# Kernel tuning notes

Measured on AMD Instinct MI355X. Metric: run time of the kernel, lower is better.

The kernel has to match this reference:

```python
import jax, jax.numpy as jnp
import numpy as np

G, K = 4, 3
P = K * K  # n_offset_points


def _conv(x, w, b, groups=1):
    # x: [B,C,H,W] NCHW, w: [O, I/groups, kh, kw] (torch OIHW), padding=1 -> SAME
    y = jax.lax.conv_general_dilated(x, w, (1, 1), 'SAME', feature_group_count=groups)
    return y + b[None, :, None, None]


def setup_inputs() -> dict:
    key = jax.random.key(0)
    ks = jax.random.split(key, 9)
    B, C, H, W = 4, 256, 64, 64
    Cg = C // G
    s = 0.05
    return {
        'x': jax.random.normal(ks[0], (B, H * W, C), jnp.float32),
        'off_w1': jax.random.normal(ks[1], (C, Cg, 3, 3), jnp.float32) * s,
        'off_b1': jax.random.normal(ks[2], (C,), jnp.float32) * s,
        'off_w2': jax.random.normal(ks[3], (G * 2 * P, C, 3, 3), jnp.float32) * s,
        'off_b2': jax.random.normal(ks[4], (G * 2 * P,), jnp.float32) * s,
        'mod_w1': jax.random.normal(ks[5], (C // 4, C, 3, 3), jnp.float32) * s,
        'mod_b1': jax.random.normal(ks[6], (C // 4,), jnp.float32) * s,
        'mod_w2': jax.random.normal(ks[7], (G * P, C // 4, 3, 3), jnp.float32) * s,
        'mod_b2': jax.random.normal(ks[8], (G * P,), jnp.float32) * s,
        'H': 64,
        'W': 64,
    }


def reference(x, off_w1, off_b1, off_w2, off_b2, mod_w1, mod_b1, mod_w2, mod_b2, H, W):
    B, N, C = x.shape
    Cg = C // G
    x2d = x.transpose(0, 2, 1).reshape(B, C, H, W)

    # offset branch (grouped 3x3 conv -> GELU -> 3x3 conv), offset_scale = 1.0
    h = jax.nn.gelu(_conv(x2d, off_w1, off_b1, groups=G), approximate=False)
    off = _conv(h, off_w2, off_b2).reshape(B, G, 2, P, H, W)
    # modulation branch
    m = jax.nn.gelu(_conv(x2d, mod_w1, mod_b1), approximate=False)
    mod = jax.nn.sigmoid(_conv(m, mod_w2, mod_b2)).reshape(B, G, P, H, W)

    # base kernel offsets: base[0]=x, base[1]=y, each [P]
    rv = jnp.arange(-(K - 1) // 2, (K - 1) // 2 + 1, dtype=x.dtype)
    by, bx = jnp.meshgrid(rv, rv, indexing='ij')
    bx, by = bx.reshape(P), by.reshape(P)

    yg, xg = jnp.meshgrid(jnp.arange(H, dtype=x.dtype), jnp.arange(W, dtype=x.dtype), indexing='ij')
    # sampling coords in pixel space; clamp to [-1,1] normalized (align_corners=True)
    # is exactly clamp to [0, W-1] / [0, H-1] in pixel space, and border padding
    # then never goes out of range.
    px = jnp.clip(xg + bx[:, None, None] + off[:, :, 0], 0.0, W - 1)  # [B,G,P,H,W]
    py = jnp.clip(yg + by[:, None, None] + off[:, :, 1], 0.0, H - 1)

    x0f, y0f = jnp.floor(px), jnp.floor(py)
    wx, wy = px - x0f, py - y0f
    x0 = x0f.astype(jnp.int32)
    y0 = y0f.astype(jnp.int32)
    x1 = jnp.minimum(x0 + 1, W - 1)
    y1 = jnp.minimum(y0 + 1, H - 1)

    flat = x2d.reshape(B, G, Cg, H * W)

    def gather(yi, xi):
        idx = (yi * W + xi).reshape(B, G, 1, P, H * W)
        return jnp.take_along_axis(flat[:, :, :, None, :], idx, axis=-1)  # [B,G,Cg,P,HW]

    wxr = wx.reshape(B, G, 1, P, H * W)
    wyr = wy.reshape(B, G, 1, P, H * W)
    v = (gather(y0, x0) * (1 - wxr) * (1 - wyr)
         + gather(y0, x1) * wxr * (1 - wyr)
         + gather(y1, x0) * (1 - wxr) * wyr
         + gather(y1, x1) * wxr * wyr)
    v = v * mod.reshape(B, G, 1, P, H * W)
    out = v.mean(axis=3)  # average over offset points -> [B,G,Cg,HW]
    return out.reshape(B, C, H * W).transpose(0, 2, 1)
```

## Files before the change

### kernel.cpp

```cpp
#include <hip/hip_runtime.h>
#include <math.h>


#define SLAB 4369
#define AGAP 1056
#define APXS 40
#define AROW (66*APXS)

typedef __attribute__((ext_vector_type(8))) short short8;
typedef __attribute__((ext_vector_type(4))) float floatx4;

__device__ __forceinline__ unsigned short f2bf(float f) {
    unsigned u = __float_as_uint(f);
    u = (u + 0x7FFFu + ((u >> 16) & 1u)) >> 16;
    return (unsigned short)u;
}
__device__ __forceinline__ float bf2f(unsigned short h) {
    return __uint_as_float(((unsigned)h) << 16);
}
__device__ __forceinline__ void split2(float v, unsigned short* hi, unsigned short* lo) {
    unsigned short h = f2bf(v);
    *hi = h;
    *lo = f2bf(v - bf2f(h));
}
__device__ __forceinline__ float gelu_exact(float v) {
    return 0.5f * v * (1.0f + erff(v * 0.70710678118654752f));
}

template<int NC, int TG, int MT, int NT, int ACT, int OUTMODE>
__device__ __forceinline__ void conv_core_lds(
    unsigned short* lds,
    const unsigned short* __restrict__ ah, const unsigned short* __restrict__ al,
    int aC0,
    const unsigned short* __restrict__ wh, const unsigned short* __restrict__ wl,
    int wC0,
    const float* __restrict__ bias,
    int b, int mblock, int tap0,
    unsigned short* __restrict__ oh, unsigned short* __restrict__ ol,
    int oC0,
    float* __restrict__ pf)
{
    const int OCPAD = NT * 16;
    const int NSTG = NC * TG;
    const int AHALF_ = MT * AROW;
    const int AU = MT * 66 * 4;
    const int KA = (AU + 255) / 256;
    const int BHALF_ = 3 * OCPAD * APXS;
    const int BU = 3 * OCPAD * 4;
    const int KB = (BU + 255) / 256;

    unsigned short* Ahl = lds;
    unsigned short* All = lds + AHALF_;
    unsigned short* Bhl = lds + 2 * AHALF_;
    unsigned short* Bll = Bhl + BHALF_;

    int tid = (int)threadIdx.x;
    int wave = tid >> 6;
    int lane = tid & 63;
    int quad = lane >> 4;
    int l16 = lane & 15;

    int pix0 = (mblock * 4 + wave) * (MT * 16);
    int y0 = mblock * MT;
    int lr = (MT == 4) ? wave : (wave >> 1);
    int xb_ = (MT == 4) ? 0 : ((wave & 1) * 32);

    floatx4 acc[MT][NT];
#pragma unroll
    for (int nt = 0; nt < NT; nt++) {
        float bv = (OUTMODE == 1) ? bias[nt * 16 + l16] : 0.f;
#pragma unroll
        for (int mt = 0; mt < MT; mt++) { floatx4 v = {bv, bv, bv, bv}; acc[mt][nt] = v; }
    }

    short8 ARh[KA], ARl[KA], BRh[KB], BRl[KB];

    auto issueAB = [&](int s) {
        int ch = s / TG;
        int kh = (TG == 3) ? (s % 3) : (tap0 / 3);
        size_t ga = ((size_t)((aC0 + ch) * 4 + b) * SLAB + (size_t)(y0 + kh) * 66) * 32;
#pragma unroll
        for (int k = 0; k < KA; k++) {
            int u = k * 256 + tid;
            if (u < AU) {
                ARh[k] = *(const short8*)(ah + ga + (size_t)u * 8);
                ARl[k] = *(const short8*)(al + ga + (size_t)u * 8);
            }
        }
        size_t gb = ((size_t)((wC0 + ch) * 9 + kh * 3)) * OCPAD * 32;
#pragma unroll
        for (int k = 0; k < KB; k++) {
            int u = k * 256 + tid;
            if (u < BU) {
                BRh[k] = *(const short8*)(wh + gb + (size_t)u * 8);
                BRl[k] = *(const short8*)(wl + gb + (size_t)u * 8);
            }
        }
    };
    auto writeAB = [&]() {
#pragma unroll
        for (int k = 0; k < KA; k++) {
            int u = k * 256 + tid;
            if (u < AU) {
                int px = u >> 2, j = u & 3;
                int row = px / 66, col = px - row * 66;
                int dst = row * AROW + col * APXS + j * 8;
                *(short8*)(Ahl + dst) = ARh[k];
                *(short8*)(All + dst) = ARl[k];
            }
        }
#pragma unroll
        for (int k = 0; k < KB; k++) {
            int u = k * 256 + tid;
            if (u < BU) {
                int tp = u / (OCPAD * 4);
                int r = u - tp * (OCPAD * 4);
                int oc = r >> 2, j = u & 3;
                int dst = tp * (OCPAD * APXS) + oc * APXS + j * 8;
                *(short8*)(Bhl + dst) = BRh[k];
                *(short8*)(Bll + dst) = BRl[k];
            }
        }
    };

    issueAB(0);
    writeAB();
    __syncthreads();

#pragma unroll 1
    for (int s = 0; s < NSTG; s++) {
        if (s + 1 < NSTG) {
            issueAB(s + 1);
            __builtin_amdgcn_sched_barrier(0);
        }
#pragma unroll
        for (int kw = 0; kw < 3; kw++) {
            short8 Afh[MT], Afl[MT], Bfh[NT], Bfl[NT];
#pragma unroll
            for (int mt = 0; mt < MT; mt++) {
                int aoff = lr * AROW + (xb_ + kw + l16 + mt * 16) * APXS + quad * 8;
                Afh[mt] = *(const short8*)(Ahl + aoff);
                Afl[mt] = *(const short8*)(All + aoff);
            }
#pragma unroll
            for (int nt = 0; nt < NT; nt++) {
                int boff = kw * (OCPAD * APXS) + (nt * 16 + l16) * APXS + quad * 8;
                Bfh[nt] = *(const short8*)(Bhl + boff);
                Bfl[nt] = *(const short8*)(Bll + boff);
            }
            __builtin_amdgcn_s_setprio(1);
#pragma unroll
            for (int nt = 0; nt < NT; nt++) {
#pragma unroll
                for (int mt = 0; mt < MT; mt++) {
                    acc[mt][nt] = __builtin_amdgcn_mfma_f32_16x16x32_bf16(Afh[mt], Bfh[nt], acc[mt][nt], 0, 0, 0);
                    acc[mt][nt] = __builtin_amdgcn_mfma_f32_16x16x32_bf16(Afh[mt], Bfl[nt], acc[mt][nt], 0, 0, 0);
                    acc[mt][nt] = __builtin_amdgcn_mfma_f32_16x16x32_bf16(Afl[mt], Bfh[nt], acc[mt][nt], 0, 0, 0);
                }
            }
            __builtin_amdgcn_s_setprio(0);
        }
        if (s + 1 < NSTG) {
            __syncthreads();
            writeAB();
            __syncthreads();
        }
    }

#pragma unroll
    for (int nt = 0; nt < NT; nt++) {
        int oc = nt * 16 + l16;
#pragma unroll
        for (int mt = 0; mt < MT; mt++) {
#pragma unroll
            for (int r = 0; r < 4; r++) {
                float v = acc[mt][nt][r];
                int px = pix0 + mt * 16 + quad * 4 + r;
                if (OUTMODE == 2) {
                    atomicAdd(pf + ((size_t)b * 4096 + px) * OCPAD + oc, v);
                } else if (OUTMODE == 3) {
                    pf[((size_t)b * 4096 + px) * OCPAD + oc] = v;
                } else {
                    if (ACT == 1) v = gelu_exact(v);
                    else if (ACT == 2) v = 1.0f / (1.0f + expf(-v));
                    int yy = (px >> 6) + 1, xx = (px & 63) + 1;
                    int och = oC0 + (oc >> 5);
                    size_t o = ((size_t)(och * 4 + b) * SLAB + yy * 66 + xx) * 32 + (oc & 31);
                    unsigned short hv, lv; split2(v, &hv, &lv);
                    oh[o] = hv; ol[o] = lv;
                }
            }
        }
    }
}

__global__ __launch_bounds__(256, 1) void convA_kernel(
    const unsigned short* __restrict__ xph, const unsigned short* __restrict__ xpl,
    const unsigned short* __restrict__ w1h, const unsigned short* __restrict__ w1l,
    const float* __restrict__ off_b1,
    const unsigned short* __restrict__ w3h, const unsigned short* __restrict__ w3l,
    unsigned short* __restrict__ h1h, unsigned short* __restrict__ h1l,
    float* __restrict__ P3)
{
    __shared__ unsigned short lds[25920];
    int bx = blockIdx.x;
    int xcd = bx & 7;
    int j = bx >> 3;
    int pair = xcd * 16 + j / 7;
    int role = j % 7;
    int mb = pair & 31;
    int b = pair >> 5;
    if (role < 4) {
        int g = role;
        conv_core_lds<2, 3, 2, 4, 1, 1>(lds, xph, xpl, g * 2,
            w1h + (size_t)g * 2 * 9 * 64 * 32, w1l + (size_t)g * 2 * 9 * 64 * 32, 0,
            off_b1 + g * 64,
            b, mb, 0, h1h, h1l, g * 2, nullptr);
    } else {
        int ks = role - 4;
        conv_core_lds<8, 1, 2, 4, 0, 2>(lds, xph, xpl, 0,
            w3h, w3l, 0, nullptr,
            b, mb, ks * 3, nullptr, nullptr, 0, P3);
    }
}

__global__ __launch_bounds__(256) void finalizeA_kernel(
    const float* __restrict__ P3, const float* __restrict__ mod_b1,
    unsigned short* __restrict__ m1h, unsigned short* __restrict__ m1l)
{
    int idx = blockIdx.x * 256 + threadIdx.x;
    int c = idx & 63;
    int p = idx >> 6;
    int b = p >> 12;
    int px = p & 4095;
    int rem = ((px >> 6) + 1) * 66 + (px & 63) + 1;
    float u = P3[(size_t)p * 64 + c] + mod_b1[c];
    u = gelu_exact(u);
    size_t o = ((size_t)((c >> 5) * 4 + b) * SLAB + rem) * 32 + (c & 31);
    unsigned short hu, lu; split2(u, &hu, &lu);
    m1h[o] = hu; m1l[o] = lu;
}

__global__ __launch_bounds__(256, 1) void convB_kernel(
    const unsigned short* __restrict__ h1h, const unsigned short* __restrict__ h1l,
    const unsigned short* __restrict__ w2h, const unsigned short* __restrict__ w2l,
    const unsigned short* __restrict__ m1h, const unsigned short* __restrict__ m1l,
    const unsigned short* __restrict__ w4h, const unsigned short* __restrict__ w4l,
    float* __restrict__ P2a, float* __restrict__ P4a)
{
    __shared__ unsigned short lds[29760];
    int bx = blockIdx.x;
    int xcd = bx & 7;
    int j = bx >> 3;
    int pair = xcd * 16 + j / 4;
    int role = j % 4;
    int mb = pair & 31;
    int b = pair >> 5;
    if (role < 3) {
        conv_core_lds<8, 1, 2, 5, 0, 2>(lds, h1h, h1l, 0,
            w2h, w2l, 0, nullptr,
            b, mb, role * 3, nullptr, nullptr, 0, P2a);
    } else {
        conv_core_lds<2, 3, 2, 3, 0, 3>(lds, m1h, m1l, 0,
            w4h, w4l, 0, nullptr,
            b, mb, 0, nullptr, nullptr, 0, P4a);
    }
}

#define ZBLK 2304
#define RBLK 1040
#define XBLK 17424
#define WBLK 1980
__global__ void prep_all_kernel(
    const float* __restrict__ x,
    const float* __restrict__ w1f, const float* __restrict__ w2f,
    const float* __restrict__ w3f, const float* __restrict__ w4f,
    unsigned short* __restrict__ xph, unsigned short* __restrict__ xpl,
    unsigned short* __restrict__ h1h, unsigned short* __restrict__ h1l,
    unsigned short* __restrict__ m1h, unsigned short* __restrict__ m1l,
    unsigned short* __restrict__ w1h, unsigned short* __restrict__ w1l,
    unsigned short* __restrict__ w2h, unsigned short* __restrict__ w2l,
    unsigned short* __restrict__ w3h, unsigned short* __restrict__ w3l,
    unsigned short* __restrict__ w4h, unsigned short* __restrict__ w4l,
    float* __restrict__ accf)
{
    int blk = blockIdx.x;
    int t = threadIdx.x;
    if (blk < ZBLK) {
        ((uint4*)accf)[(size_t)blk * 256 + t] = make_uint4(0u, 0u, 0u, 0u);
        return;
    }
    blk -= ZBLK;
    if (blk < RBLK) {
        int b = blk / 260;
        int r = blk - b * 260;
        int i, j;
        if (r < 66)       { i = 0;        j = r; }
        else if (r < 132) { i = 65;       j = r - 66; }
        else if (r < 196) { i = r - 131;  j = 0; }
        else              { i = r - 195;  j = 65; }
        size_t pp = (size_t)i * 66 + j;
        int ch = t >> 5, sub = t & 31;
        size_t o = ((size_t)(ch * 4 + b) * SLAB + pp) * 32 + sub;
        h1h[o] = 0; h1l[o] = 0;
        if (t < 64) { m1h[o] = 0; m1l[o] = 0; }
        return;
    }
    blk -= RBLK;
    if (blk < XBLK) {
        int b = blk / 4356;
        int rem = blk - b * 4356;
        int i = rem / 66, j = rem - i * 66;
        float v = 0.f;
        if (i >= 1 && i <= 64 && j >= 1 && j <= 64)
            v = x[((size_t)b * 4096 + (size_t)(i - 1) * 64 + (j - 1)) * 256 + t];
        size_t o = ((size_t)((t >> 5) * 4 + b) * SLAB + rem) * 32 + (t & 31);
        unsigned short h, l; split2(v, &h, &l);
        xph[o] = h; xpl[o] = l;
        return;
    }
    blk -= XBLK;
    {
        const int N1 = 147456, N2 = 184320, N3 = 147456, N4 = 27648;
        int idx = blk * 256 + t;
        const float* w; unsigned short *outh, *outl;
        int ocpad, oc_real, ic, base;
        if (idx < N1)                { w = w1f; outh = w1h; outl = w1l; ocpad = 64; oc_real = 64; ic = 64;  base = 0; }
        else if (idx < N1 + N2)      { w = w2f; outh = w2h; outl = w2l; ocpad = 80; oc_real = 72; ic = 256; base = N1; }
        else if (idx < N1 + N2 + N3) { w = w3f; outh = w3h; outl = w3l; ocpad = 64; oc_real = 64; ic = 256; base = N1 + N2; }
        else                         { w = w4f; outh = w4h; outl = w4l; ocpad = 48; oc_real = 36; ic = 64;  base = N1 + N2 + N3; }
        int lidx = idx - base;
        int ici = lidx & 31;
        int t1 = lidx >> 5;
        int ocp = t1 % ocpad;
        int t2 = t1 / ocpad;
        int tap = t2 % 9;
        int t3 = t2 / 9;
        int nch = ic >> 5;
        int ch = t3 % nch;
        int g = t3 / nch;
        float v = 0.f;
        if (ocp < oc_real) {
            int oc = g * oc_real + ocp;
            int icx = ch * 32 + ici;
            v = w[((size_t)oc * ic + icx) * 9 + tap];
        }
        unsigned short h, l; split2(v, &h, &l);
        outh[lidx] = h; outl[lidx] = l;
    }
}

__global__ __launch_bounds__(256) void deform_sample(
    const float* __restrict__ x,
    const float* __restrict__ P2a, const float* __restrict__ P4a,
    const float* __restrict__ b2, const float* __restrict__ b4,
    float* __restrict__ out)
{
    int bid = (int)((blockIdx.x & 7u) * 512u + (blockIdx.x >> 3));
    int wid = (int)(((unsigned)bid * 256u + threadIdx.x) >> 6);
    int lane = (int)(threadIdx.x & 63u);
    int sub = lane >> 4;
    int li = lane & 15;

    int b = wid >> 12;
    int rem = wid & 4095;
    int g = rem >> 10;
    int hw = ((rem & 1023) << 2) + sub;
    int hy = hw >> 6;
    int wx = hw & 63;

    float fx = 0.f, fy = 0.f, fm = 0.f;
    if (li < 9) {
        size_t p = (size_t)(b << 12) + hw;
        int c2 = g * 18 + li;
        fx = P2a[p * 80 + c2] + b2[c2];
        fy = P2a[p * 80 + 9 + c2] + b2[9 + c2];
        int c4 = g * 9 + li;
        float mv = P4a[p * 48 + c4] + b4[c4];
        fm = 1.0f / (1.0f + expf(-mv));
    }
    float px = fminf(fmaxf((float)wx + (float)(li % 3 - 1) + fx, 0.f), 63.f);
    float py = fminf(fmaxf((float)hy + (float)(li / 3 - 1) + fy, 0.f), 63.f);
    float x0f = floorf(px), y0f = floorf(py);
    float wxf = px - x0f, wyf = py - y0f;
    int x0 = (int)x0f, y0 = (int)y0f;
    int x1 = min(x0 + 1, 63), y1 = min(y0 + 1, 63);

    const float4* xb = (const float4*)(x + ((size_t)(b << 12)) * 256 + g * 64 + li * 4);
    float4 acc = make_float4(0.f, 0.f, 0.f, 0.f);
    int sb = sub << 4;
#pragma unroll
    for (int q = 0; q < 9; q++) {
        int src = sb + q;
        int   qx0 = __shfl(x0, src);
        int   qx1 = __shfl(x1, src);
        int   qy0 = __shfl(y0, src);
        int   qy1 = __shfl(y1, src);
        float qwx = __shfl(wxf, src);
        float qwy = __shfl(wyf, src);
        float qm  = __shfl(fm, src);
        float4 v00 = xb[(size_t)(qy0 * 64 + qx0) * 64];
        float4 v01 = xb[(size_t)(qy0 * 64 + qx1) * 64];
        float4 v10 = xb[(size_t)(qy1 * 64 + qx0) * 64];
        float4 v11 = xb[(size_t)(qy1 * 64 + qx1) * 64];
        float w00 = (1.f - qwx) * (1.f - qwy);
        float w01 = qwx * (1.f - qwy);
        float w10 = (1.f - qwx) * qwy;
        float w11 = qwx * qwy;
        acc.x += qm * (v00.x * w00 + v01.x * w01 + v10.x * w10 + v11.x * w11);
        acc.y += qm * (v00.y * w00 + v01.y * w01 + v10.y * w10 + v11.y * w11);
        acc.z += qm * (v00.z * w00 + v01.z * w01 + v10.z * w10 + v11.z * w11);
        acc.w += qm * (v00.w * w00 + v01.w * w01 + v10.w * w10 + v11.w * w11);
    }
    const float s = 1.f / 9.f;
    acc.x *= s; acc.y *= s; acc.z *= s; acc.w *= s;
    float4* ob = (float4*)(out + ((size_t)(b << 12) + hw) * 256 + g * 64 + li * 4);
    *ob = acc;
}

extern "C" void kernel_launch(void* const* d_in, const int* in_sizes, int n_in,
                              void* d_out, int out_size, void* d_ws, size_t ws_size,
                              hipStream_t stream)
{
    const float* x      = (const float*)d_in[0];
    const float* off_w1 = (const float*)d_in[1];
    const float* off_b1 = (const float*)d_in[2];
    const float* off_w2 = (const float*)d_in[3];
    const float* off_b2 = (const float*)d_in[4];
    const float* mod_w1 = (const float*)d_in[5];
    const float* mod_b1 = (const float*)d_in[6];
    const float* mod_w2 = (const float*)d_in[7];
    const float* mod_b2 = (const float*)d_in[8];

    const size_t XP = 8u * 4u * SLAB * 32u;
    const size_t MP = 2u * 4u * SLAB * 32u;
    const size_t W1 = 4u * 2u * 9u * 64u * 32u;
    const size_t W2 = 8u * 9u * 80u * 32u;
    const size_t W3 = 8u * 9u * 64u * 32u;
    const size_t W4 = 2u * 9u * 48u * 32u;

    unsigned short* ws = (unsigned short*)d_ws;
    size_t o = 0;
    unsigned short* xph = ws + o; o += XP + AGAP;
    unsigned short* xpl = ws + o; o += XP + AGAP;
    unsigned short* h1h = ws + o; o += XP + AGAP;
    unsigned short* h1l = ws + o; o += XP + AGAP;
    unsigned short* m1h = ws + o; o += MP + AGAP;
    unsigned short* m1l = ws + o; o += MP + AGAP;
    unsigned short* w1h = ws + o; o += W1 + AGAP;
    unsigned short* w1l = ws + o; o += W1 + AGAP;
    unsigned short* w2h = ws + o; o += W2 + AGAP;
    unsigned short* w2l = ws + o; o += W2 + AGAP;
    unsigned short* w3h = ws + o; o += W3 + AGAP;
    unsigned short* w3l = ws + o; o += W3 + AGAP;
    unsigned short* w4h = ws + o; o += W4 + AGAP;
    unsigned short* w4l = ws + o; o += W4 + AGAP;
    o += o & 1;
    float* fbase = (float*)(ws + o);
    float* P3  = fbase;
    float* P2a = P3 + (size_t)4 * 4096 * 64;
    float* P4a = P2a + (size_t)4 * 4096 * 80;
    const size_t ACC_FLOATS = (size_t)4 * 4096 * (64 + 80 + 48);
    size_t need_bytes = o * 2 + ACC_FLOATS * 4;
    if (ws_size < need_bytes) return;

    prep_all_kernel<<<ZBLK + RBLK + XBLK + WBLK, 256, 0, stream>>>(
        x, off_w1, off_w2, mod_w1, mod_w2,
        xph, xpl, h1h, h1l, m1h, m1l,
        w1h, w1l, w2h, w2l, w3h, w3l, w4h, w4l, P3);

    convA_kernel<<<dim3(896, 1, 1), 256, 0, stream>>>(xph, xpl, w1h, w1l, off_b1,
                                                      w3h, w3l, h1h, h1l, P3);
    finalizeA_kernel<<<4096, 256, 0, stream>>>(P3, mod_b1, m1h, m1l);
    convB_kernel<<<dim3(512, 1, 1), 256, 0, stream>>>(h1h, h1l, w2h, w2l,
                                                      m1h, m1l, w4h, w4l, P2a, P4a);
    deform_sample<<<4096, 256, 0, stream>>>(x, P2a, P4a, off_b2, mod_b2, (float*)d_out);
}
```

Baseline: 190.2 us.

## Split convolutions over output channels instead of kernel rows, dropping atomics and finalize

The convolutions no longer split the 3x3 kernel rows across blocks and combine partial sums with fp32 atomics. Each block now covers all nine taps for a slice of output channels and writes its result directly, with bias and GELU fused in. This removes the accumulator zeroing in the prep kernel, the atomic traffic, and the separate finalize kernel, and shrinks the grids of both conv launches. In exchange, each block runs a longer serial K loop with fewer blocks in flight, which may lower occupancy and load balance.

```diff
diff --git a/kernel.cpp b/kernel.cpp
--- a/kernel.cpp
+++ b/kernel.cpp
@@ -27,7 +27,7 @@
     return 0.5f * v * (1.0f + erff(v * 0.70710678118654752f));
 }
 
-template<int NC, int TG, int MT, int NT, int ACT, int OUTMODE>
+template<int NC, int MT, int NT, int OCW, int OSTRF, int ACT, int OUTMODE>
 __device__ __forceinline__ void conv_core_lds(
     unsigned short* lds,
     const unsigned short* __restrict__ ah, const unsigned short* __restrict__ al,
@@ -35,18 +35,19 @@
     const unsigned short* __restrict__ wh, const unsigned short* __restrict__ wl,
     int wC0,
     const float* __restrict__ bias,
-    int b, int mblock, int tap0,
+    int b, int mblock,
     unsigned short* __restrict__ oh, unsigned short* __restrict__ ol,
     int oC0,
-    float* __restrict__ pf)
-{
-    const int OCPAD = NT * 16;
-    const int NSTG = NC * TG;
+    float* __restrict__ pf,
+    int oc0)
+{
+    const int NSTG = NC * 3;
     const int AHALF_ = MT * AROW;
     const int AU = MT * 66 * 4;
     const int KA = (AU + 255) / 256;
-    const int BHALF_ = 3 * OCPAD * APXS;
-    const int BU = 3 * OCPAD * 4;
+    const int BHALF_ = 3 * NT * 16 * APXS;
+    const int UB1 = NT * 64;
+    const int BU = 3 * UB1;
     const int KB = (BU + 255) / 256;
 
     unsigned short* Ahl = lds;
@@ -62,8 +63,8 @@
 
     int pix0 = (mblock * 4 + wave) * (MT * 16);
     int y0 = mblock * MT;
-    int lr = (MT == 4) ? wave : (wave >> 1);
-    int xb_ = (MT == 4) ? 0 : ((wave & 1) * 32);
+    int lr = wave >> 1;
+    int xb_ = (wave & 1) * 32;
 
     floatx4 acc[MT][NT];
 #pragma unroll
@@ -76,8 +77,8 @@
     short8 ARh[KA], ARl[KA], BRh[KB], BRl[KB];
 
     auto issueAB = [&](int s) {
-        int ch = s / TG;
-        int kh = (TG == 3) ? (s % 3) : (tap0 / 3);
+        int ch = s / 3;
+        int kh = s % 3;
         size_t ga = ((size_t)((aC0 + ch) * 4 + b) * SLAB + (size_t)(y0 + kh) * 66) * 32;
 #pragma unroll
         for (int k = 0; k < KA; k++) {
@@ -87,13 +88,16 @@
                 ARl[k] = *(const short8*)(al + ga + (size_t)u * 8);
             }
         }
-        size_t gb = ((size_t)((wC0 + ch) * 9 + kh * 3)) * OCPAD * 32;
+        size_t gb = (((size_t)(wC0 + ch) * 9 + kh * 3) * OCW + oc0) * 32;
 #pragma unroll
         for (int k = 0; k < KB; k++) {
             int u = k * 256 + tid;
             if (u < BU) {
-                BRh[k] = *(const short8*)(wh + gb + (size_t)u * 8);
-                BRl[k] = *(const short8*)(wl + gb + (size_t)u * 8);
+                int tp = u / UB1;
+                int r = u - tp * UB1;
+                size_t src = gb + (size_t)tp * OCW * 32 + (size_t)r * 8;
+                BRh[k] = *(const short8*)(wh + src);
+                BRl[k] = *(const short8*)(wl + src);
             }
         }
     };
@@ -113,10 +117,9 @@
         for (int k = 0; k < KB; k++) {
             int u = k * 256 + tid;
             if (u < BU) {
-                int tp = u / (OCPAD * 4);
-                int r = u - tp * (OCPAD * 4);
-                int oc = r >> 2, j = u & 3;
-                int dst = tp * (OCPAD * APXS) + oc * APXS + j * 8;
+                int tp = u / UB1;
+                int r = u - tp * UB1;
+                int dst = tp * (NT * 16 * APXS) + (r >> 2) * APXS + (r & 3) * 8;
                 *(short8*)(Bhl + dst) = BRh[k];
                 *(short8*)(Bll + dst) = BRl[k];
             }
@@ -144,7 +147,7 @@
             }
 #pragma unroll
             for (int nt = 0; nt < NT; nt++) {
-                int boff = kw * (OCPAD * APXS) + (nt * 16 + l16) * APXS + quad * 8;
+                int boff = kw * (NT * 16 * APXS) + (nt * 16 + l16) * APXS + quad * 8;
                 Bfh[nt] = *(const short8*)(Bhl + boff);
                 Bfl[nt] = *(const short8*)(Bll + boff);
             }
@@ -176,16 +179,14 @@
             for (int r = 0; r < 4; r++) {
                 float v = acc[mt][nt][r];
                 int px = pix0 + mt * 16 + quad * 4 + r;
-                if (OUTMODE == 2) {
-                    atomicAdd(pf + ((size_t)b * 4096 + px) * OCPAD + oc, v);
-                } else if (OUTMODE == 3) {
-                    pf[((size_t)b * 4096 + px) * OCPAD + oc] = v;
+                if (OUTMODE == 3) {
+                    pf[((size_t)b * 4096 + px) * OSTRF + oc0 + oc] = v;
                 } else {
                     if (ACT == 1) v = gelu_exact(v);
-                    else if (ACT == 2) v = 1.0f / (1.0f + expf(-v));
                     int yy = (px >> 6) + 1, xx = (px & 63) + 1;
-                    int och = oC0 + (oc >> 5);
-                    size_t o = ((size_t)(och * 4 + b) * SLAB + yy * 66 + xx) * 32 + (oc & 31);
+                    int oca = oc0 + oc;
+                    int och = oC0 + (oca >> 5);
+                    size_t o = ((size_t)(och * 4 + b) * SLAB + yy * 66 + xx) * 32 + (oca & 31);
                     unsigned short hv, lv; split2(v, &hv, &lv);
                     oh[o] = hv; ol[o] = lv;
                 }
@@ -199,46 +200,33 @@
     const unsigned short* __restrict__ w1h, const unsigned short* __restrict__ w1l,
     const float* __restrict__ off_b1,
     const unsigned short* __restrict__ w3h, const unsigned short* __restrict__ w3l,
+    const float* __restrict__ mod_b1,
     unsigned short* __restrict__ h1h, unsigned short* __restrict__ h1l,
-    float* __restrict__ P3)
+    unsigned short* __restrict__ m1h, unsigned short* __restrict__ m1l)
 {
     __shared__ unsigned short lds[25920];
     int bx = blockIdx.x;
     int xcd = bx & 7;
     int j = bx >> 3;
-    int pair = xcd * 16 + j / 7;
-    int role = j % 7;
-    int mb = pair & 31;
-    int b = pair >> 5;
-    if (role < 4) {
-        int g = role;
-        conv_core_lds<2, 3, 2, 4, 1, 1>(lds, xph, xpl, g * 2,
+    if (j < 32) {
+        int ocr = j & 1;
+        int pair = xcd * 16 + (j >> 1);
+        int mb = pair & 31;
+        int b = pair >> 5;
+        conv_core_lds<8, 2, 2, 64, 0, 1, 1>(lds, xph, xpl, 0,
+            w3h, w3l, 0, mod_b1 + ocr * 32,
+            b, mb, m1h, m1l, 0, nullptr, ocr * 32);
+    } else {
+        int jj = j - 32;
+        int g = jj & 3;
+        int pair = xcd * 16 + (jj >> 2);
+        int mb = pair & 31;
+        int b = pair >> 5;
+        conv_core_lds<2, 2, 4, 64, 0, 1, 1>(lds, xph, xpl, g * 2,
             w1h + (size_t)g * 2 * 9 * 64 * 32, w1l + (size_t)g * 2 * 9 * 64 * 32, 0,
             off_b1 + g * 64,
-            b, mb, 0, h1h, h1l, g * 2, nullptr);
-    } else {
-        int ks = role - 4;
-        conv_core_lds<8, 1, 2, 4, 0, 2>(lds, xph, xpl, 0,
-            w3h, w3l, 0, nullptr,
-            b, mb, ks * 3, nullptr, nullptr, 0, P3);
-    }
-}
-
-__global__ __launch_bounds__(256) void finalizeA_kernel(
-    const float* __restrict__ P3, const float* __restrict__ mod_b1,
-    unsigned short* __restrict__ m1h, unsigned short* __restrict__ m1l)
-{
-    int idx = blockIdx.x * 256 + threadIdx.x;
-    int c = idx & 63;
-    int p = idx >> 6;
-    int b = p >> 12;
-    int px = p & 4095;
-    int rem = ((px >> 6) + 1) * 66 + (px & 63) + 1;
-    float u = P3[(size_t)p * 64 + c] + mod_b1[c];
-    u = gelu_exact(u);
-    size_t o = ((size_t)((c >> 5) * 4 + b) * SLAB + rem) * 32 + (c & 31);
-    unsigned short hu, lu; split2(u, &hu, &lu);
-    m1h[o] = hu; m1l[o] = lu;
+            b, mb, h1h, h1l, g * 2, nullptr, 0);
+    }
 }
 
 __global__ __launch_bounds__(256, 1) void convB_kernel(
@@ -248,26 +236,31 @@
     const unsigned short* __restrict__ w4h, const unsigned short* __restrict__ w4l,
     float* __restrict__ P2a, float* __restrict__ P4a)
 {
-    __shared__ unsigned short lds[29760];
+    __shared__ unsigned short lds[22080];
     int bx = blockIdx.x;
     int xcd = bx & 7;
     int j = bx >> 3;
-    int pair = xcd * 16 + j / 4;
-    int role = j % 4;
-    int mb = pair & 31;
-    int b = pair >> 5;
-    if (role < 3) {
-        conv_core_lds<8, 1, 2, 5, 0, 2>(lds, h1h, h1l, 0,
-            w2h, w2l, 0, nullptr,
-            b, mb, role * 3, nullptr, nullptr, 0, P2a);
+    if (j < 32) {
+        int ocr = j & 1;
+        int pair = xcd * 16 + (j >> 1);
+        int mb = pair & 31;
+        int b = pair >> 5;
+        if (ocr == 0) {
+            conv_core_lds<8, 2, 3, 80, 80, 0, 3>(lds, h1h, h1l, 0,
+                w2h, w2l, 0, nullptr, b, mb, nullptr, nullptr, 0, P2a, 0);
+        } else {
+            conv_core_lds<8, 2, 2, 80, 80, 0, 3>(lds, h1h, h1l, 0,
+                w2h, w2l, 0, nullptr, b, mb, nullptr, nullptr, 0, P2a, 48);
+        }
     } else {
-        conv_core_lds<2, 3, 2, 3, 0, 3>(lds, m1h, m1l, 0,
-            w4h, w4l, 0, nullptr,
-            b, mb, 0, nullptr, nullptr, 0, P4a);
-    }
-}
-
-#define ZBLK 2304
+        int pair = xcd * 16 + (j - 32);
+        int mb = pair & 31;
+        int b = pair >> 5;
+        conv_core_lds<2, 2, 3, 48, 48, 0, 3>(lds, m1h, m1l, 0,
+            w4h, w4l, 0, nullptr, b, mb, nullptr, nullptr, 0, P4a, 0);
+    }
+}
+
 #define RBLK 1040
 #define XBLK 17424
 #define WBLK 1980
@@ -281,16 +274,10 @@
     unsigned short* __restrict__ w1h, unsigned short* __restrict__ w1l,
     unsigned short* __restrict__ w2h, unsigned short* __restrict__ w2l,
     unsigned short* __restrict__ w3h, unsigned short* __restrict__ w3l,
-    unsigned short* __restrict__ w4h, unsigned short* __restrict__ w4l,
-    float* __restrict__ accf)
+    unsigned short* __restrict__ w4h, unsigned short* __restrict__ w4l)
 {
     int blk = blockIdx.x;
     int t = threadIdx.x;
-    if (blk < ZBLK) {
-        ((uint4*)accf)[(size_t)blk * 256 + t] = make_uint4(0u, 0u, 0u, 0u);
-        return;
-    }
-    blk -= ZBLK;
     if (blk < RBLK) {
         int b = blk / 260;
         int r = blk - b * 260;
@@ -457,22 +444,21 @@
     unsigned short* w4l = ws + o; o += W4 + AGAP;
     o += o & 1;
     float* fbase = (float*)(ws + o);
-    float* P3  = fbase;
-    float* P2a = P3 + (size_t)4 * 4096 * 64;
+    float* P2a = fbase;
     float* P4a = P2a + (size_t)4 * 4096 * 80;
-    const size_t ACC_FLOATS = (size_t)4 * 4096 * (64 + 80 + 48);
+    const size_t ACC_FLOATS = (size_t)4 * 4096 * (80 + 48);
     size_t need_bytes = o * 2 + ACC_FLOATS * 4;
     if (ws_size < need_bytes) return;
 
-    prep_all_kernel<<<ZBLK + RBLK + XBLK + WBLK, 256, 0, stream>>>(
+    prep_all_kernel<<<RBLK + XBLK + WBLK, 256, 0, stream>>>(
         x, off_w1, off_w2, mod_w1, mod_w2,
         xph, xpl, h1h, h1l, m1h, m1l,
-        w1h, w1l, w2h, w2l, w3h, w3l, w4h, w4l, P3);
-
-    convA_kernel<<<dim3(896, 1, 1), 256, 0, stream>>>(xph, xpl, w1h, w1l, off_b1,
-                                                      w3h, w3l, h1h, h1l, P3);
-    finalizeA_kernel<<<4096, 256, 0, stream>>>(P3, mod_b1, m1h, m1l);
-    convB_kernel<<<dim3(512, 1, 1), 256, 0, stream>>>(h1h, h1l, w2h, w2l,
+        w1h, w1l, w2h, w2l, w3h, w3l, w4h, w4l);
+
+    convA_kernel<<<dim3(768, 1, 1), 256, 0, stream>>>(xph, xpl, w1h, w1l, off_b1,
+                                                      w3h, w3l, mod_b1,
+                                                      h1h, h1l, m1h, m1l);
+    convB_kernel<<<dim3(384, 1, 1), 256, 0, stream>>>(h1h, h1l, w2h, w2l,
                                                       m1h, m1l, w4h, w4l, P2a, P4a);
     deform_sample<<<4096, 256, 0, stream>>>(x, P2a, P4a, off_b2, mod_b2, (float*)d_out);
 }
```

Measured after the change: 182.3 us. -4.2%, faster.
